# Performance work log

Hardware: AMD Instinct MI355X
Metric: run time of the kernel (lower is better)

## Reference

```python
import jax, jax.numpy as jnp
import numpy as np

B, T, F1, F2 = 16384, 5, 300, 251
IN, H = 551, 128

def setup_inputs() -> dict:
    key = jax.random.key(0)
    ks = jax.random.split(key, 16)
    s = 0.05
    return {
        "x1": jax.random.normal(ks[0], (B, T, F1), jnp.float32),
        "x2": jax.random.normal(ks[1], (B, T, F2), jnp.float32),
        "W_ih": jax.random.normal(ks[2], (4 * H, IN), jnp.float32) * s,
        "W_hh": jax.random.normal(ks[3], (4 * H, H), jnp.float32) * s,
        "b_ih": jax.random.normal(ks[4], (4 * H,), jnp.float32) * s,
        "b_hh": jax.random.normal(ks[5], (4 * H,), jnp.float32) * s,
        "W1": jax.random.normal(ks[6], (531, H * T), jnp.float32) * s,
        "b1": jax.random.normal(ks[7], (531,), jnp.float32) * s,
        "W2": jax.random.normal(ks[8], (256, 531), jnp.float32) * s,
        "b2": jax.random.normal(ks[9], (256,), jnp.float32) * s,
        "W3": jax.random.normal(ks[10], (64, 256), jnp.float32) * s,
        "b3": jax.random.normal(ks[11], (64,), jnp.float32) * s,
        "W4": jax.random.normal(ks[12], (2, 64), jnp.float32) * s,
        "b4": jax.random.normal(ks[13], (2,), jnp.float32) * s,
    }

def _lstm(x, W_ih, W_hh, b_ih, b_hh):
    # x: [B, T, IN] -> outputs [B, T, H]; PyTorch gate order i, f, g, o
    xg = jnp.einsum('bti,gi->btg', x, W_ih) + b_ih + b_hh  # [B, T, 4H]
    xg = jnp.transpose(xg, (1, 0, 2))  # [T, B, 4H]
    h0 = jnp.zeros((x.shape[0], H), x.dtype)
    c0 = jnp.zeros((x.shape[0], H), x.dtype)

    def step(carry, xg_t):
        h, c = carry
        g = xg_t + h @ W_hh.T  # [B, 4H]
        i, f, gg, o = jnp.split(g, 4, axis=-1)
        c = jax.nn.sigmoid(f) * c + jax.nn.sigmoid(i) * jnp.tanh(gg)
        h = jax.nn.sigmoid(o) * jnp.tanh(c)
        return (h, c), h

    _, hs = jax.lax.scan(step, (h0, c0), xg)  # hs: [T, B, H]
    return jnp.transpose(hs, (1, 0, 2))

def reference(x1, x2, W_ih, W_hh, b_ih, b_hh, W1, b1, W2, b2, W3, b3, W4, b4):
    x = jnp.concatenate((x1, x2), axis=2)  # [B, T, 551]
    h = _lstm(x, W_ih, W_hh, b_ih, b_hh)   # [B, T, H]
    h = h.reshape(h.shape[0], T * H)
    h = jax.nn.relu(h @ W1.T + b1)
    h = jax.nn.relu(h @ W2.T + b2)
    h = jax.nn.relu(h @ W3.T + b3)
    logits = h @ W4.T + b4
    return jax.nn.softmax(logits, axis=1)
```

## Files before the change

### kernel.cpp

```cpp
#include <hip/hip_runtime.h>
#include <hip/hip_bf16.h>


typedef short  short8  __attribute__((ext_vector_type(8)));
typedef short  short4v __attribute__((ext_vector_type(4)));
typedef float  f32x4   __attribute__((ext_vector_type(4)));

#define MFMA(a, b, c) __builtin_amdgcn_mfma_f32_16x16x32_bf16((a), (b), (c), 0, 0, 0)

__device__ __forceinline__ short f2bs(float f) {
    __hip_bfloat16 h = __float2bfloat16(f);
    union { __hip_bfloat16 h; short s; } u; u.h = h; return u.s;
}
__device__ __forceinline__ float b2f(short s) {
    union { unsigned u; float f; } v; v.u = ((unsigned)(unsigned short)s) << 16; return v.f;
}
__device__ __forceinline__ float sigf(float x)  { return 1.f / (1.f + __expf(-x)); }
__device__ __forceinline__ float mytanh(float x){ return 2.f / (1.f + __expf(-2.f * x)) - 1.f; }

#define BB     16384
#define TT     5
#define F1     300
#define F2     251
#define INF    551
#define KP     576
#define G4     512
#define HH     128
#define FLAT   640
#define L1N    531
#define L1P    576
#define L1KP   544
#define L2N    256
#define L3N    64

#define O_WIH  0u
#define O_WHH  589824u
#define O_W1   720896u
#define O_W2   1458176u
#define O_W3   1736704u
#define O_BG   1769472u
#define O_B1   1771520u
#define O_XG   1773824u
#define O_HS   85659904u
#define WS_NEED 106631424u

__device__ __forceinline__ void pack_b(const float* __restrict__ W, short* __restrict__ dst,
                                       int i, int tpn, int Nsrc, int Ksrc, int ldw)
{
    int tile = i >> 9, rem = i & 511, lane = rem >> 3, jj = rem & 7;
    int tn = tile / tpn, tk = tile - tn * tpn;
    int n = tn * 16 + (lane & 15);
    int k = tk * 32 + (lane >> 4) * 8 + jj;
    float v = (n < Nsrc && k < Ksrc) ? W[n * ldw + k] : 0.f;
    dst[i] = f2bs(v);
}

__global__ void prep_kernel(
    const float* __restrict__ W_ih, const float* __restrict__ W_hh,
    const float* __restrict__ b_ih, const float* __restrict__ b_hh,
    const float* __restrict__ W1,   const float* __restrict__ b1,
    const float* __restrict__ W2,   const float* __restrict__ W3,
    short* __restrict__ Wihp, short* __restrict__ Whhp, float* __restrict__ biasg,
    short* __restrict__ W1p,  float* __restrict__ b1p,  short* __restrict__ W2p,
    short* __restrict__ W3p)
{
    const int N0 = G4 * KP;
    const int N1 = N0 + G4 * HH;
    const int N2 = N1 + L1P * FLAT;
    const int N3 = N2 + L2N * L1KP;
    const int N4 = N3 + L3N * L2N;
    const int N5 = N4 + G4;
    const int N6 = N5 + L1P;
    const int stride = gridDim.x * blockDim.x;
    for (int i = blockIdx.x * blockDim.x + threadIdx.x; i < N6; i += stride) {
        if (i < N0)      pack_b(W_ih, Wihp, i,       18, G4,  INF, INF);
        else if (i < N1) pack_b(W_hh, Whhp, i - N0,   4, G4,  HH,  HH);
        else if (i < N2) pack_b(W1,   W1p,  i - N1,  20, L1N, FLAT, FLAT);
        else if (i < N3) pack_b(W2,   W2p,  i - N2,  17, L2N, L1N, L1N);
        else if (i < N4) pack_b(W3,   W3p,  i - N3,   8, L3N, L2N, L2N);
        else if (i < N5) { int j = i - N4; biasg[j] = b_ih[j] + b_hh[j]; }
        else             { int j = i - N5; b1p[j] = (j < L1N) ? b1[j] : 0.f; }
    }
}

__device__ __forceinline__ float4 load_chunk4(const float* __restrict__ x1,
                                              const float* __restrict__ x2,
                                              int brow, int t, int c)
{
    if (c < F1) {
        return *(const float4*)(x1 + (brow * TT + t) * F1 + c);
    }
    float4 r;
    int base = (brow * TT + t) * F2 + (c - F1);
    r.x = (c + 0 < INF) ? x2[base + 0] : 0.f;
    r.y = (c + 1 < INF) ? x2[base + 1] : 0.f;
    r.z = (c + 2 < INF) ? x2[base + 2] : 0.f;
    r.w = (c + 3 < INF) ? x2[base + 3] : 0.f;
    return r;
}

__global__ __launch_bounds__(512, 4) void k1_xgemm(
    const float* __restrict__ x1, const float* __restrict__ x2,
    const short* __restrict__ Wihp, const float* __restrict__ biasg,
    short* __restrict__ xg)
{
    __shared__ __align__(16) short At[64][296];
    const int tid  = threadIdx.x;
    const int w    = tid >> 6;
    const int lane = tid & 63;
    const int quad = lane >> 4;
    const int c16  = lane & 15;
    const int m0   = blockIdx.x * 64;
    const int t    = m0 >> 14;
    const int bb   = m0 & 16383;

    f32x4 acc[4][4];
#pragma unroll
    for (int mt = 0; mt < 4; ++mt)
#pragma unroll
        for (int nt = 0; nt < 4; ++nt)
            acc[mt][nt] = (f32x4){0.f, 0.f, 0.f, 0.f};

    const int srow  = tid >> 3;
    const int kslot = tid & 7;

    for (int half = 0; half < 2; ++half) {
        __syncthreads();
        {
            int brow = bb + srow;
#pragma unroll
            for (int c = 0; c < 9; ++c) {
                int kl = c * 32 + kslot * 4;
                float4 v = load_chunk4(x1, x2, brow, t, half * 288 + kl);
                short4v s;
                s[0] = f2bs(v.x); s[1] = f2bs(v.y); s[2] = f2bs(v.z); s[3] = f2bs(v.w);
                *(short4v*)&At[srow][kl] = s;
            }
        }
        __syncthreads();
#pragma unroll
        for (int ks = 0; ks < 9; ++ks) {
            short8 a[4];
#pragma unroll
            for (int mt = 0; mt < 4; ++mt)
                a[mt] = *(const short8*)&At[mt * 16 + c16][ks * 32 + quad * 8];
#pragma unroll
            for (int nt = 0; nt < 4; ++nt) {
                int tk = half * 9 + ks;
                short8 b = *(const short8*)&Wihp[(((w * 4 + nt) * 18 + tk) << 9) + lane * 8];
#pragma unroll
                for (int mt = 0; mt < 4; ++mt)
                    acc[mt][nt] = MFMA(a[mt], b, acc[mt][nt]);
            }
        }
    }
#pragma unroll
    for (int nt = 0; nt < 4; ++nt) {
        float bv = biasg[w * 64 + nt * 16 + c16];
#pragma unroll
        for (int mt = 0; mt < 4; ++mt) {
            short4v o;
#pragma unroll
            for (int r = 0; r < 4; ++r) o[r] = f2bs(acc[mt][nt][r] + bv);
            int tm = (m0 >> 4) + mt, tn = w * 4 + nt;
            *(short4v*)&xg[((tm * 32 + tn) << 8) + lane * 4] = o;
        }
    }
}

__global__ __launch_bounds__(512, 2) void k2_rec(
    const short* __restrict__ Whhp, const short* __restrict__ xg,
    short* __restrict__ hs)
{
    __shared__ __align__(16) short hb[2][32][136];
    const int tid  = threadIdx.x;
    const int w    = tid >> 6;
    const int lane = tid & 63;
    const int quad = lane >> 4;
    const int c16  = lane & 15;
    const int btile = blockIdx.x * 2;

    short8 bfr[4][4];
#pragma unroll
    for (int g = 0; g < 4; ++g)
#pragma unroll
        for (int ks = 0; ks < 4; ++ks)
            bfr[g][ks] = *(const short8*)&Whhp[((((g * 8 + w) * 4) + ks) << 9) + lane * 8];

    float cst[2][4];
#pragma unroll
    for (int mt = 0; mt < 2; ++mt)
#pragma unroll
        for (int r = 0; r < 4; ++r) cst[mt][r] = 0.f;

    const int j = w * 16 + c16;

    for (int t = 0; t < TT; ++t) {
        short4v xq[2][4];
#pragma unroll
        for (int mt = 0; mt < 2; ++mt)
#pragma unroll
            for (int g = 0; g < 4; ++g)
                xq[mt][g] = *(const short4v*)
                    &xg[((((t << 10) + btile + mt) * 32 + (g * 8 + w)) << 8) + lane * 4];

        f32x4 acc[2][4];
#pragma unroll
        for (int mt = 0; mt < 2; ++mt)
#pragma unroll
            for (int g = 0; g < 4; ++g)
                acc[mt][g] = (f32x4){0.f, 0.f, 0.f, 0.f};

        if (t > 0) {
            const short (*cur)[136] = hb[(t - 1) & 1];
#pragma unroll
            for (int ks = 0; ks < 4; ++ks) {
                short8 a[2];
#pragma unroll
                for (int mt = 0; mt < 2; ++mt)
                    a[mt] = *(const short8*)&cur[mt * 16 + c16][ks * 32 + quad * 8];
#pragma unroll
                for (int mt = 0; mt < 2; ++mt)
#pragma unroll
                    for (int g = 0; g < 4; ++g)
                        acc[mt][g] = MFMA(a[mt], bfr[g][ks], acc[mt][g]);
            }
        }

        short (*nxt)[136] = hb[t & 1];
#pragma unroll
        for (int mt = 0; mt < 2; ++mt) {
#pragma unroll
            for (int r = 0; r < 4; ++r) {
                int m = mt * 16 + quad * 4 + r;
                float gi = acc[mt][0][r] + b2f(xq[mt][0][r]);
                float gf = acc[mt][1][r] + b2f(xq[mt][1][r]);
                float gg = acc[mt][2][r] + b2f(xq[mt][2][r]);
                float go = acc[mt][3][r] + b2f(xq[mt][3][r]);
                float cn = sigf(gf) * cst[mt][r] + sigf(gi) * mytanh(gg);
                cst[mt][r] = cn;
                nxt[m][j] = f2bs(sigf(go) * mytanh(cn));
            }
        }
        __syncthreads();
        {
            int tm = w >> 2, kt = w & 3;
            short8 v = *(const short8*)&nxt[tm * 16 + c16][kt * 32 + quad * 8];
            *(short8*)&hs[(((btile + tm) * 20 + t * 4 + kt) << 9) + lane * 8] = v;
        }
    }
}

__global__ __launch_bounds__(256, 2) void mlp_kernel(
    const short* __restrict__ hs,
    const short* __restrict__ W1p, const float* __restrict__ b1p,
    const short* __restrict__ W2p, const float* __restrict__ b2,
    const short* __restrict__ W3p, const float* __restrict__ b3,
    const float* __restrict__ W4,  const float* __restrict__ b4,
    float* __restrict__ out)
{
    __shared__ __align__(16) short a1[32][584];
    __shared__ __align__(16) short a2[32][264];
    __shared__ __align__(16) short a3[32][72];
    const int tid  = threadIdx.x;
    const int w    = tid >> 6;
    const int lane = tid & 63;
    const int quad = lane >> 4;
    const int c16  = lane & 15;
    const int m0   = blockIdx.x * 32;
    const int mtile = blockIdx.x * 2;

    {
        f32x4 acc[2][9];
#pragma unroll
        for (int mt = 0; mt < 2; ++mt)
#pragma unroll
            for (int i = 0; i < 9; ++i)
                acc[mt][i] = (f32x4){0.f, 0.f, 0.f, 0.f};
#pragma unroll 4
        for (int ks = 0; ks < 20; ++ks) {
            short8 a[2];
#pragma unroll
            for (int mt = 0; mt < 2; ++mt)
                a[mt] = *(const short8*)&hs[(((mtile + mt) * 20 + ks) << 9) + lane * 8];
#pragma unroll
            for (int i = 0; i < 9; ++i) {
                short8 b = *(const short8*)&W1p[(((w * 9 + i) * 20 + ks) << 9) + lane * 8];
                acc[0][i] = MFMA(a[0], b, acc[0][i]);
                acc[1][i] = MFMA(a[1], b, acc[1][i]);
            }
        }
#pragma unroll
        for (int i = 0; i < 9; ++i) {
            int n = (w * 9 + i) * 16 + c16;
            float bv = b1p[n];
#pragma unroll
            for (int mt = 0; mt < 2; ++mt)
#pragma unroll
                for (int r = 0; r < 4; ++r) {
                    int m = mt * 16 + quad * 4 + r;
                    float v = acc[mt][i][r] + bv;
                    a1[m][n] = f2bs(v > 0.f ? v : 0.f);
                }
        }
    }
    __syncthreads();

    {
        f32x4 acc[2][4];
#pragma unroll
        for (int mt = 0; mt < 2; ++mt)
#pragma unroll
            for (int i = 0; i < 4; ++i)
                acc[mt][i] = (f32x4){0.f, 0.f, 0.f, 0.f};
#pragma unroll 4
        for (int ks = 0; ks < 17; ++ks) {
            short8 a[2];
#pragma unroll
            for (int mt = 0; mt < 2; ++mt)
                a[mt] = *(const short8*)&a1[mt * 16 + c16][ks * 32 + quad * 8];
#pragma unroll
            for (int i = 0; i < 4; ++i) {
                short8 b = *(const short8*)&W2p[(((w * 4 + i) * 17 + ks) << 9) + lane * 8];
                acc[0][i] = MFMA(a[0], b, acc[0][i]);
                acc[1][i] = MFMA(a[1], b, acc[1][i]);
            }
        }
#pragma unroll
        for (int i = 0; i < 4; ++i) {
            int n = (w * 4 + i) * 16 + c16;
            float bv = b2[n];
#pragma unroll
            for (int mt = 0; mt < 2; ++mt)
#pragma unroll
                for (int r = 0; r < 4; ++r) {
                    int m = mt * 16 + quad * 4 + r;
                    float v = acc[mt][i][r] + bv;
                    a2[m][n] = f2bs(v > 0.f ? v : 0.f);
                }
        }
    }
    __syncthreads();

    {
        f32x4 acc[2];
        acc[0] = (f32x4){0.f, 0.f, 0.f, 0.f};
        acc[1] = (f32x4){0.f, 0.f, 0.f, 0.f};
#pragma unroll
        for (int ks = 0; ks < 8; ++ks) {
            short8 a[2];
#pragma unroll
            for (int mt = 0; mt < 2; ++mt)
                a[mt] = *(const short8*)&a2[mt * 16 + c16][ks * 32 + quad * 8];
            short8 b = *(const short8*)&W3p[((w * 8 + ks) << 9) + lane * 8];
            acc[0] = MFMA(a[0], b, acc[0]);
            acc[1] = MFMA(a[1], b, acc[1]);
        }
        int n = w * 16 + c16;
        float bv = b3[n];
#pragma unroll
        for (int mt = 0; mt < 2; ++mt)
#pragma unroll
            for (int r = 0; r < 4; ++r) {
                int m = mt * 16 + quad * 4 + r;
                float v = acc[mt][r] + bv;
                a3[m][n] = f2bs(v > 0.f ? v : 0.f);
            }
    }
    __syncthreads();

    if (tid < 64) {
        int m   = tid >> 1;
        int cls = tid & 1;
        float s = b4[cls];
#pragma unroll 8
        for (int k = 0; k < 64; ++k)
            s += b2f(a3[m][k]) * W4[cls * 64 + k];
        float other = __shfl_xor(s, 1);
        float p = 1.f / (1.f + __expf(other - s));
        out[(m0 + m) * 2 + cls] = p;
    }
}

extern "C" void kernel_launch(void* const* d_in, const int* in_sizes, int n_in,
                              void* d_out, int out_size, void* d_ws, size_t ws_size,
                              hipStream_t stream)
{
    (void)in_sizes; (void)n_in; (void)out_size;
    if (ws_size < (size_t)WS_NEED) return;

    const float* x1   = (const float*)d_in[0];
    const float* x2   = (const float*)d_in[1];
    const float* W_ih = (const float*)d_in[2];
    const float* W_hh = (const float*)d_in[3];
    const float* b_ih = (const float*)d_in[4];
    const float* b_hh = (const float*)d_in[5];
    const float* W1   = (const float*)d_in[6];
    const float* b1   = (const float*)d_in[7];
    const float* W2   = (const float*)d_in[8];
    const float* b2   = (const float*)d_in[9];
    const float* W3   = (const float*)d_in[10];
    const float* b3   = (const float*)d_in[11];
    const float* W4   = (const float*)d_in[12];
    const float* b4   = (const float*)d_in[13];

    char* ws = (char*)d_ws;
    short* Wihp  = (short*)(ws + O_WIH);
    short* Whhp  = (short*)(ws + O_WHH);
    short* W1p   = (short*)(ws + O_W1);
    short* W2p   = (short*)(ws + O_W2);
    short* W3p   = (short*)(ws + O_W3);
    float* biasg = (float*)(ws + O_BG);
    float* b1p   = (float*)(ws + O_B1);
    short* xg    = (short*)(ws + O_XG);
    short* hsb   = (short*)(ws + O_HS);

    prep_kernel<<<3461, 256, 0, stream>>>(W_ih, W_hh, b_ih, b_hh, W1, b1, W2, W3,
                                          Wihp, Whhp, biasg, W1p, b1p, W2p, W3p);
    k1_xgemm<<<1280, 512, 0, stream>>>(x1, x2, Wihp, biasg, xg);
    k2_rec<<<512, 512, 0, stream>>>(Whhp, xg, hsb);
    mlp_kernel<<<512, 256, 0, stream>>>(hsb, W1p, b1p, W2p, b2, W3p, b3, W4, b4,
                                        (float*)d_out);
}
```

Baseline: 354.9 us.

## Fuse input GEMM, LSTM recurrence and MLP into a single kernel

Replaces the three kernels (input projection GEMM, recurrence, MLP) with one kernel per 32-row batch tile. The input projection is computed on the fly from fp32 x1/x2 loaded straight into MFMA fragments, and hidden states stay in shared memory for the MLP. This removes the large bf16 xg and hs round trips through global memory and two launches. In exchange, the input GEMM now runs on only 512 blocks with less reuse of the W_ih fragments, and its global loads are uncoalesced per-row float4 reads. The MLP also moves from 256 to 512 threads per block.

```diff
diff --git a/kernel.cpp b/kernel.cpp
--- a/kernel.cpp
+++ b/kernel.cpp
@@ -3,7 +3,6 @@
 
 
 typedef short  short8  __attribute__((ext_vector_type(8)));
-typedef short  short4v __attribute__((ext_vector_type(4)));
 typedef float  f32x4   __attribute__((ext_vector_type(4)));
 
 #define MFMA(a, b, c) __builtin_amdgcn_mfma_f32_16x16x32_bf16((a), (b), (c), 0, 0, 0)
@@ -18,20 +17,16 @@
 __device__ __forceinline__ float sigf(float x)  { return 1.f / (1.f + __expf(-x)); }
 __device__ __forceinline__ float mytanh(float x){ return 2.f / (1.f + __expf(-2.f * x)) - 1.f; }
 
-#define BB     16384
 #define TT     5
 #define F1     300
 #define F2     251
 #define INF    551
-#define KP     576
 #define G4     512
 #define HH     128
 #define FLAT   640
 #define L1N    531
-#define L1P    576
 #define L1KP   544
 #define L2N    256
-#define L3N    64
 
 #define O_WIH  0u
 #define O_WHH  589824u
@@ -40,9 +35,16 @@
 #define O_W3   1736704u
 #define O_BG   1769472u
 #define O_B1   1771520u
-#define O_XG   1773824u
-#define O_HS   85659904u
-#define WS_NEED 106631424u
+#define WS_NEED 1773824u
+
+#define SM_TOTAL 39424
+#define AFL_STR  648
+#define A1_OFF   20736
+#define A1_STR   584
+#define A2_OFF   0
+#define A2_STR   264
+#define A3_OFF   8448
+#define A3_STR   72
 
 __device__ __forceinline__ void pack_b(const float* __restrict__ W, short* __restrict__ dst,
                                        int i, int tpn, int Nsrc, int Ksrc, int ldw)
@@ -64,297 +66,256 @@
     short* __restrict__ W1p,  float* __restrict__ b1p,  short* __restrict__ W2p,
     short* __restrict__ W3p)
 {
-    const int N0 = G4 * KP;
+    const int N0 = G4 * 576;
     const int N1 = N0 + G4 * HH;
-    const int N2 = N1 + L1P * FLAT;
+    const int N2 = N1 + 576 * FLAT;
     const int N3 = N2 + L2N * L1KP;
-    const int N4 = N3 + L3N * L2N;
+    const int N4 = N3 + 64 * L2N;
     const int N5 = N4 + G4;
-    const int N6 = N5 + L1P;
+    const int N6 = N5 + 576;
     const int stride = gridDim.x * blockDim.x;
     for (int i = blockIdx.x * blockDim.x + threadIdx.x; i < N6; i += stride) {
         if (i < N0)      pack_b(W_ih, Wihp, i,       18, G4,  INF, INF);
         else if (i < N1) pack_b(W_hh, Whhp, i - N0,   4, G4,  HH,  HH);
         else if (i < N2) pack_b(W1,   W1p,  i - N1,  20, L1N, FLAT, FLAT);
         else if (i < N3) pack_b(W2,   W2p,  i - N2,  17, L2N, L1N, L1N);
-        else if (i < N4) pack_b(W3,   W3p,  i - N3,   8, L3N, L2N, L2N);
+        else if (i < N4) pack_b(W3,   W3p,  i - N3,   8, 64,  L2N, L2N);
         else if (i < N5) { int j = i - N4; biasg[j] = b_ih[j] + b_hh[j]; }
         else             { int j = i - N5; b1p[j] = (j < L1N) ? b1[j] : 0.f; }
     }
 }
 
-__device__ __forceinline__ float4 load_chunk4(const float* __restrict__ x1,
-                                              const float* __restrict__ x2,
-                                              int brow, int t, int c)
-{
-    if (c < F1) {
-        return *(const float4*)(x1 + (brow * TT + t) * F1 + c);
-    }
-    float4 r;
-    int base = (brow * TT + t) * F2 + (c - F1);
-    r.x = (c + 0 < INF) ? x2[base + 0] : 0.f;
-    r.y = (c + 1 < INF) ? x2[base + 1] : 0.f;
-    r.z = (c + 2 < INF) ? x2[base + 2] : 0.f;
-    r.w = (c + 3 < INF) ? x2[base + 3] : 0.f;
-    return r;
-}
-
-__global__ __launch_bounds__(512, 4) void k1_xgemm(
+__global__ __launch_bounds__(512, 2) void fused_kernel(
     const float* __restrict__ x1, const float* __restrict__ x2,
-    const short* __restrict__ Wihp, const float* __restrict__ biasg,
-    short* __restrict__ xg)
-{
-    __shared__ __align__(16) short At[64][296];
-    const int tid  = threadIdx.x;
-    const int w    = tid >> 6;
-    const int lane = tid & 63;
-    const int quad = lane >> 4;
-    const int c16  = lane & 15;
-    const int m0   = blockIdx.x * 64;
-    const int t    = m0 >> 14;
-    const int bb   = m0 & 16383;
-
-    f32x4 acc[4][4];
-#pragma unroll
-    for (int mt = 0; mt < 4; ++mt)
-#pragma unroll
-        for (int nt = 0; nt < 4; ++nt)
-            acc[mt][nt] = (f32x4){0.f, 0.f, 0.f, 0.f};
-
-    const int srow  = tid >> 3;
-    const int kslot = tid & 7;
-
-    for (int half = 0; half < 2; ++half) {
-        __syncthreads();
-        {
-            int brow = bb + srow;
-#pragma unroll
-            for (int c = 0; c < 9; ++c) {
-                int kl = c * 32 + kslot * 4;
-                float4 v = load_chunk4(x1, x2, brow, t, half * 288 + kl);
-                short4v s;
-                s[0] = f2bs(v.x); s[1] = f2bs(v.y); s[2] = f2bs(v.z); s[3] = f2bs(v.w);
-                *(short4v*)&At[srow][kl] = s;
-            }
-        }
-        __syncthreads();
-#pragma unroll
-        for (int ks = 0; ks < 9; ++ks) {
-            short8 a[4];
-#pragma unroll
-            for (int mt = 0; mt < 4; ++mt)
-                a[mt] = *(const short8*)&At[mt * 16 + c16][ks * 32 + quad * 8];
-#pragma unroll
-            for (int nt = 0; nt < 4; ++nt) {
-                int tk = half * 9 + ks;
-                short8 b = *(const short8*)&Wihp[(((w * 4 + nt) * 18 + tk) << 9) + lane * 8];
-#pragma unroll
-                for (int mt = 0; mt < 4; ++mt)
-                    acc[mt][nt] = MFMA(a[mt], b, acc[mt][nt]);
-            }
-        }
-    }
-#pragma unroll
-    for (int nt = 0; nt < 4; ++nt) {
-        float bv = biasg[w * 64 + nt * 16 + c16];
-#pragma unroll
-        for (int mt = 0; mt < 4; ++mt) {
-            short4v o;
-#pragma unroll
-            for (int r = 0; r < 4; ++r) o[r] = f2bs(acc[mt][nt][r] + bv);
-            int tm = (m0 >> 4) + mt, tn = w * 4 + nt;
-            *(short4v*)&xg[((tm * 32 + tn) << 8) + lane * 4] = o;
-        }
-    }
-}
-
-__global__ __launch_bounds__(512, 2) void k2_rec(
-    const short* __restrict__ Whhp, const short* __restrict__ xg,
-    short* __restrict__ hs)
-{
-    __shared__ __align__(16) short hb[2][32][136];
-    const int tid  = threadIdx.x;
-    const int w    = tid >> 6;
-    const int lane = tid & 63;
-    const int quad = lane >> 4;
-    const int c16  = lane & 15;
-    const int btile = blockIdx.x * 2;
-
-    short8 bfr[4][4];
-#pragma unroll
-    for (int g = 0; g < 4; ++g)
-#pragma unroll
-        for (int ks = 0; ks < 4; ++ks)
-            bfr[g][ks] = *(const short8*)&Whhp[((((g * 8 + w) * 4) + ks) << 9) + lane * 8];
-
-    float cst[2][4];
-#pragma unroll
-    for (int mt = 0; mt < 2; ++mt)
-#pragma unroll
-        for (int r = 0; r < 4; ++r) cst[mt][r] = 0.f;
-
-    const int j = w * 16 + c16;
-
-    for (int t = 0; t < TT; ++t) {
-        short4v xq[2][4];
-#pragma unroll
-        for (int mt = 0; mt < 2; ++mt)
-#pragma unroll
-            for (int g = 0; g < 4; ++g)
-                xq[mt][g] = *(const short4v*)
-                    &xg[((((t << 10) + btile + mt) * 32 + (g * 8 + w)) << 8) + lane * 4];
-
-        f32x4 acc[2][4];
-#pragma unroll
-        for (int mt = 0; mt < 2; ++mt)
-#pragma unroll
-            for (int g = 0; g < 4; ++g)
-                acc[mt][g] = (f32x4){0.f, 0.f, 0.f, 0.f};
-
-        if (t > 0) {
-            const short (*cur)[136] = hb[(t - 1) & 1];
-#pragma unroll
-            for (int ks = 0; ks < 4; ++ks) {
-                short8 a[2];
-#pragma unroll
-                for (int mt = 0; mt < 2; ++mt)
-                    a[mt] = *(const short8*)&cur[mt * 16 + c16][ks * 32 + quad * 8];
-#pragma unroll
-                for (int mt = 0; mt < 2; ++mt)
-#pragma unroll
-                    for (int g = 0; g < 4; ++g)
-                        acc[mt][g] = MFMA(a[mt], bfr[g][ks], acc[mt][g]);
-            }
-        }
-
-        short (*nxt)[136] = hb[t & 1];
-#pragma unroll
-        for (int mt = 0; mt < 2; ++mt) {
-#pragma unroll
-            for (int r = 0; r < 4; ++r) {
-                int m = mt * 16 + quad * 4 + r;
-                float gi = acc[mt][0][r] + b2f(xq[mt][0][r]);
-                float gf = acc[mt][1][r] + b2f(xq[mt][1][r]);
-                float gg = acc[mt][2][r] + b2f(xq[mt][2][r]);
-                float go = acc[mt][3][r] + b2f(xq[mt][3][r]);
-                float cn = sigf(gf) * cst[mt][r] + sigf(gi) * mytanh(gg);
-                cst[mt][r] = cn;
-                nxt[m][j] = f2bs(sigf(go) * mytanh(cn));
-            }
-        }
-        __syncthreads();
-        {
-            int tm = w >> 2, kt = w & 3;
-            short8 v = *(const short8*)&nxt[tm * 16 + c16][kt * 32 + quad * 8];
-            *(short8*)&hs[(((btile + tm) * 20 + t * 4 + kt) << 9) + lane * 8] = v;
-        }
-    }
-}
-
-__global__ __launch_bounds__(256, 2) void mlp_kernel(
-    const short* __restrict__ hs,
+    const short* __restrict__ Wihp, const short* __restrict__ Whhp,
+    const float* __restrict__ biasg,
     const short* __restrict__ W1p, const float* __restrict__ b1p,
     const short* __restrict__ W2p, const float* __restrict__ b2,
     const short* __restrict__ W3p, const float* __restrict__ b3,
     const float* __restrict__ W4,  const float* __restrict__ b4,
     float* __restrict__ out)
 {
-    __shared__ __align__(16) short a1[32][584];
-    __shared__ __align__(16) short a2[32][264];
-    __shared__ __align__(16) short a3[32][72];
+    __shared__ __align__(16) short sA[SM_TOTAL];
     const int tid  = threadIdx.x;
     const int w    = tid >> 6;
     const int lane = tid & 63;
     const int quad = lane >> 4;
     const int c16  = lane & 15;
-    const int m0   = blockIdx.x * 32;
-    const int mtile = blockIdx.x * 2;
+    const int b0   = blockIdx.x * 32;
+    const int j    = w * 16 + c16;
+
+    float bg[4];
+#pragma unroll
+    for (int g = 0; g < 4; ++g) bg[g] = biasg[g * HH + j];
+
+    short8 whh[4][4];
+#pragma unroll
+    for (int g = 0; g < 4; ++g)
+#pragma unroll
+        for (int ks = 0; ks < 4; ++ks)
+            whh[g][ks] = *(const short8*)&Whhp[((((g * 8 + w) * 4) + ks) << 9) + lane * 8];
+
+    float cst[2][4];
+#pragma unroll
+    for (int mt = 0; mt < 2; ++mt)
+#pragma unroll
+        for (int r = 0; r < 4; ++r) cst[mt][r] = 0.f;
+
+    for (int t = 0; t < TT; ++t) {
+        const float* x1r[2];
+        const float* x2r[2];
+#pragma unroll
+        for (int mt = 0; mt < 2; ++mt) {
+            int brow = b0 + mt * 16 + c16;
+            x1r[mt] = x1 + (brow * TT + t) * F1;
+            x2r[mt] = x2 + (brow * TT + t) * F2;
+        }
+
+        f32x4 acc[2][4];
+#pragma unroll
+        for (int mt = 0; mt < 2; ++mt)
+#pragma unroll
+            for (int g = 0; g < 4; ++g)
+                acc[mt][g] = (f32x4){0.f, 0.f, 0.f, 0.f};
+
+        float4 cur0[2], cur1[2];
+#pragma unroll
+        for (int mt = 0; mt < 2; ++mt) {
+            int k0 = quad * 8;
+            cur0[mt] = (k0     < F1) ? *(const float4*)(x1r[mt] + k0)
+                                     : *(const float4*)(x2r[mt] + (k0 - F1));
+            cur1[mt] = (k0 + 4 < F1) ? *(const float4*)(x1r[mt] + k0 + 4)
+                                     : *(const float4*)(x2r[mt] + (k0 + 4 - F1));
+        }
+        for (int tk = 0; tk < 17; ++tk) {
+            short8 afr[2];
+#pragma unroll
+            for (int mt = 0; mt < 2; ++mt) {
+                afr[mt][0] = f2bs(cur0[mt].x); afr[mt][1] = f2bs(cur0[mt].y);
+                afr[mt][2] = f2bs(cur0[mt].z); afr[mt][3] = f2bs(cur0[mt].w);
+                afr[mt][4] = f2bs(cur1[mt].x); afr[mt][5] = f2bs(cur1[mt].y);
+                afr[mt][6] = f2bs(cur1[mt].z); afr[mt][7] = f2bs(cur1[mt].w);
+            }
+            if (tk < 16) {
+#pragma unroll
+                for (int mt = 0; mt < 2; ++mt) {
+                    int k0 = (tk + 1) * 32 + quad * 8;
+                    cur0[mt] = (k0     < F1) ? *(const float4*)(x1r[mt] + k0)
+                                             : *(const float4*)(x2r[mt] + (k0 - F1));
+                    cur1[mt] = (k0 + 4 < F1) ? *(const float4*)(x1r[mt] + k0 + 4)
+                                             : *(const float4*)(x2r[mt] + (k0 + 4 - F1));
+                }
+            }
+#pragma unroll
+            for (int g = 0; g < 4; ++g) {
+                short8 bfr = *(const short8*)&Wihp[(((g * 8 + w) * 18 + tk) << 9) + lane * 8];
+                acc[0][g] = MFMA(afr[0], bfr, acc[0][g]);
+                acc[1][g] = MFMA(afr[1], bfr, acc[1][g]);
+            }
+        }
+        {
+            short8 afr[2];
+#pragma unroll
+            for (int mt = 0; mt < 2; ++mt) {
+#pragma unroll
+                for (int jj = 0; jj < 8; ++jj) {
+                    int k = 544 + quad * 8 + jj;
+                    afr[mt][jj] = (k < INF) ? f2bs(x2r[mt][k - F1]) : (short)0;
+                }
+            }
+#pragma unroll
+            for (int g = 0; g < 4; ++g) {
+                short8 bfr = *(const short8*)&Wihp[(((g * 8 + w) * 18 + 17) << 9) + lane * 8];
+                acc[0][g] = MFMA(afr[0], bfr, acc[0][g]);
+                acc[1][g] = MFMA(afr[1], bfr, acc[1][g]);
+            }
+        }
+
+        if (t > 0) {
+#pragma unroll
+            for (int ks = 0; ks < 4; ++ks) {
+                short8 ha[2];
+#pragma unroll
+                for (int mt = 0; mt < 2; ++mt)
+                    ha[mt] = *(const short8*)
+                        &sA[(mt * 16 + c16) * AFL_STR + (t - 1) * HH + ks * 32 + quad * 8];
+#pragma unroll
+                for (int g = 0; g < 4; ++g) {
+                    acc[0][g] = MFMA(ha[0], whh[g][ks], acc[0][g]);
+                    acc[1][g] = MFMA(ha[1], whh[g][ks], acc[1][g]);
+                }
+            }
+        }
+
+#pragma unroll
+        for (int mt = 0; mt < 2; ++mt) {
+#pragma unroll
+            for (int r = 0; r < 4; ++r) {
+                int m = mt * 16 + quad * 4 + r;
+                float gi = acc[mt][0][r] + bg[0];
+                float gf = acc[mt][1][r] + bg[1];
+                float gg = acc[mt][2][r] + bg[2];
+                float go = acc[mt][3][r] + bg[3];
+                float cn = sigf(gf) * cst[mt][r] + sigf(gi) * mytanh(gg);
+                cst[mt][r] = cn;
+                sA[m * AFL_STR + t * HH + j] = f2bs(sigf(go) * mytanh(cn));
+            }
+        }
+        __syncthreads();
+    }
 
     {
-        f32x4 acc[2][9];
+        const int ntc = (w < 4) ? 5 : 4;
+        f32x4 acc1[2][5];
 #pragma unroll
         for (int mt = 0; mt < 2; ++mt)
 #pragma unroll
-            for (int i = 0; i < 9; ++i)
-                acc[mt][i] = (f32x4){0.f, 0.f, 0.f, 0.f};
-#pragma unroll 4
+            for (int i = 0; i < 5; ++i)
+                acc1[mt][i] = (f32x4){0.f, 0.f, 0.f, 0.f};
         for (int ks = 0; ks < 20; ++ks) {
             short8 a[2];
 #pragma unroll
             for (int mt = 0; mt < 2; ++mt)
-                a[mt] = *(const short8*)&hs[(((mtile + mt) * 20 + ks) << 9) + lane * 8];
-#pragma unroll
-            for (int i = 0; i < 9; ++i) {
-                short8 b = *(const short8*)&W1p[(((w * 9 + i) * 20 + ks) << 9) + lane * 8];
-                acc[0][i] = MFMA(a[0], b, acc[0][i]);
-                acc[1][i] = MFMA(a[1], b, acc[1][i]);
-            }
-        }
-#pragma unroll
-        for (int i = 0; i < 9; ++i) {
-            int n = (w * 9 + i) * 16 + c16;
-            float bv = b1p[n];
+                a[mt] = *(const short8*)&sA[(mt * 16 + c16) * AFL_STR + ks * 32 + quad * 8];
+#pragma unroll
+            for (int i = 0; i < 5; ++i) {
+                if (i < ntc) {
+                    int tn = w + 8 * i;
+                    short8 b = *(const short8*)&W1p[((tn * 20 + ks) << 9) + lane * 8];
+                    acc1[0][i] = MFMA(a[0], b, acc1[0][i]);
+                    acc1[1][i] = MFMA(a[1], b, acc1[1][i]);
+                }
+            }
+        }
+        __syncthreads();
+#pragma unroll
+        for (int i = 0; i < 5; ++i) {
+            if (i < ntc) {
+                int tn = w + 8 * i;
+                int n  = tn * 16 + c16;
+                float bv = b1p[n];
+#pragma unroll
+                for (int mt = 0; mt < 2; ++mt)
+#pragma unroll
+                    for (int r = 0; r < 4; ++r) {
+                        int m = mt * 16 + quad * 4 + r;
+                        float v = acc1[mt][i][r] + bv;
+                        sA[A1_OFF + m * A1_STR + n] = f2bs(v > 0.f ? v : 0.f);
+                    }
+            }
+        }
+    }
+    __syncthreads();
+
+    {
+        f32x4 acc2[2][2];
+#pragma unroll
+        for (int mt = 0; mt < 2; ++mt)
+#pragma unroll
+            for (int i = 0; i < 2; ++i)
+                acc2[mt][i] = (f32x4){0.f, 0.f, 0.f, 0.f};
+        for (int ks = 0; ks < 17; ++ks) {
+            short8 a[2];
+#pragma unroll
+            for (int mt = 0; mt < 2; ++mt)
+                a[mt] = *(const short8*)&sA[A1_OFF + (mt * 16 + c16) * A1_STR + ks * 32 + quad * 8];
+#pragma unroll
+            for (int i = 0; i < 2; ++i) {
+                int tn = w * 2 + i;
+                short8 b = *(const short8*)&W2p[((tn * 17 + ks) << 9) + lane * 8];
+                acc2[0][i] = MFMA(a[0], b, acc2[0][i]);
+                acc2[1][i] = MFMA(a[1], b, acc2[1][i]);
+            }
+        }
+#pragma unroll
+        for (int i = 0; i < 2; ++i) {
+            int n = (w * 2 + i) * 16 + c16;
+            float bv = b2[n];
 #pragma unroll
             for (int mt = 0; mt < 2; ++mt)
 #pragma unroll
                 for (int r = 0; r < 4; ++r) {
                     int m = mt * 16 + quad * 4 + r;
-                    float v = acc[mt][i][r] + bv;
-                    a1[m][n] = f2bs(v > 0.f ? v : 0.f);
+                    float v = acc2[mt][i][r] + bv;
+                    sA[A2_OFF + m * A2_STR + n] = f2bs(v > 0.f ? v : 0.f);
                 }
         }
     }
     __syncthreads();
 
-    {
-        f32x4 acc[2][4];
-#pragma unroll
-        for (int mt = 0; mt < 2; ++mt)
-#pragma unroll
-            for (int i = 0; i < 4; ++i)
-                acc[mt][i] = (f32x4){0.f, 0.f, 0.f, 0.f};
-#pragma unroll 4
-        for (int ks = 0; ks < 17; ++ks) {
-            short8 a[2];
-#pragma unroll
-            for (int mt = 0; mt < 2; ++mt)
-                a[mt] = *(const short8*)&a1[mt * 16 + c16][ks * 32 + quad * 8];
-#pragma unroll
-            for (int i = 0; i < 4; ++i) {
-                short8 b = *(const short8*)&W2p[(((w * 4 + i) * 17 + ks) << 9) + lane * 8];
-                acc[0][i] = MFMA(a[0], b, acc[0][i]);
-                acc[1][i] = MFMA(a[1], b, acc[1][i]);
-            }
-        }
-#pragma unroll
-        for (int i = 0; i < 4; ++i) {
-            int n = (w * 4 + i) * 16 + c16;
-            float bv = b2[n];
-#pragma unroll
-            for (int mt = 0; mt < 2; ++mt)
-#pragma unroll
-                for (int r = 0; r < 4; ++r) {
-                    int m = mt * 16 + quad * 4 + r;
-                    float v = acc[mt][i][r] + bv;
-                    a2[m][n] = f2bs(v > 0.f ? v : 0.f);
-                }
-        }
-    }
-    __syncthreads();
-
-    {
-        f32x4 acc[2];
-        acc[0] = (f32x4){0.f, 0.f, 0.f, 0.f};
-        acc[1] = (f32x4){0.f, 0.f, 0.f, 0.f};
+    if (w < 4) {
+        f32x4 acc3[2];
+        acc3[0] = (f32x4){0.f, 0.f, 0.f, 0.f};
+        acc3[1] = (f32x4){0.f, 0.f, 0.f, 0.f};
 #pragma unroll
         for (int ks = 0; ks < 8; ++ks) {
             short8 a[2];
 #pragma unroll
             for (int mt = 0; mt < 2; ++mt)
-                a[mt] = *(const short8*)&a2[mt * 16 + c16][ks * 32 + quad * 8];
+                a[mt] = *(const short8*)&sA[A2_OFF + (mt * 16 + c16) * A2_STR + ks * 32 + quad * 8];
             short8 b = *(const short8*)&W3p[((w * 8 + ks) << 9) + lane * 8];
-            acc[0] = MFMA(a[0], b, acc[0]);
-            acc[1] = MFMA(a[1], b, acc[1]);
+            acc3[0] = MFMA(a[0], b, acc3[0]);
+            acc3[1] = MFMA(a[1], b, acc3[1]);
         }
         int n = w * 16 + c16;
         float bv = b3[n];
@@ -363,8 +324,8 @@
 #pragma unroll
             for (int r = 0; r < 4; ++r) {
                 int m = mt * 16 + quad * 4 + r;
-                float v = acc[mt][r] + bv;
-                a3[m][n] = f2bs(v > 0.f ? v : 0.f);
+                float v = acc3[mt][r] + bv;
+                sA[A3_OFF + m * A3_STR + n] = f2bs(v > 0.f ? v : 0.f);
             }
     }
     __syncthreads();
@@ -375,10 +336,10 @@
         float s = b4[cls];
 #pragma unroll 8
         for (int k = 0; k < 64; ++k)
-            s += b2f(a3[m][k]) * W4[cls * 64 + k];
+            s += b2f(sA[A3_OFF + m * A3_STR + k]) * W4[cls * 64 + k];
         float other = __shfl_xor(s, 1);
         float p = 1.f / (1.f + __expf(other - s));
-        out[(m0 + m) * 2 + cls] = p;
+        out[(b0 + m) * 2 + cls] = p;
     }
 }
 
@@ -412,13 +373,10 @@
     short* W3p   = (short*)(ws + O_W3);
     float* biasg = (float*)(ws + O_BG);
     float* b1p   = (float*)(ws + O_B1);
-    short* xg    = (short*)(ws + O_XG);
-    short* hsb   = (short*)(ws + O_HS);
 
     prep_kernel<<<3461, 256, 0, stream>>>(W_ih, W_hh, b_ih, b_hh, W1, b1, W2, W3,
                                           Wihp, Whhp, biasg, W1p, b1p, W2p, W3p);
-    k1_xgemm<<<1280, 512, 0, stream>>>(x1, x2, Wihp, biasg, xg);
-    k2_rec<<<512, 512, 0, stream>>>(Whhp, xg, hsb);
-    mlp_kernel<<<512, 256, 0, stream>>>(hsb, W1p, b1p, W2p, b2, W3p, b3, W4, b4,
-                                        (float*)d_out);
-}
+    fused_kernel<<<512, 512, 0, stream>>>(x1, x2, Wihp, Whhp, biasg,
+                                          W1p, b1p, W2p, b2, W3p, b3, W4, b4,
+                                          (float*)d_out);
+}
```

New measurement: 442.9 us. +24.8%, slower.
